# Performance work log

Measured on AMD Instinct MI355X. Metric: run time of the kernel, lower is better.

Reference implementation:

```python
import jax, jax.numpy as jnp
import numpy as np

jax.config.update("jax_enable_x64", True)

B, T, C = 64, 720, 512


def setup_inputs() -> dict:
    key = jax.random.key(0)
    kx, _ = jax.random.split(key)
    x = jax.random.normal(kx, (B, T, C), dtype=jnp.float32)
    # learnable EMA coefficient (scalar parameter)
    alpha = jnp.asarray(0.3, dtype=jnp.float32)
    return {"x": x, "alpha": alpha}


def reference(x, alpha):
    # x: [B, T, C] float32, alpha: scalar float32
    t = x.shape[1]
    alpha_d = alpha.astype(jnp.float64)
    # powers = flip(arange(t)) = [t-1, t-2, ..., 0], double precision as in torch
    powers = jnp.arange(t - 1, -1, -1, dtype=jnp.float64)  # [T]
    base = jnp.power(1.0 - alpha_d, powers)                # (1-a)^(t-1-i), [T]
    divisor = base
    # weights[0] = base[0]; weights[i>=1] = base[i] * alpha
    weights = base * jnp.where(jnp.arange(t) == 0, 1.0, alpha_d)
    # broadcast to [1, T, 1]; compute in float64 (torch promotes f32*f64 -> f64)
    num = jnp.cumsum(x.astype(jnp.float64) * weights[None, :, None], axis=1)
    ma = (num / divisor[None, :, None]).astype(jnp.float32)  # [B, T, C]
    res = x - ma
    return (res, ma)
```

## Files before the change

kernel.cpp:

```cpp
#include <hip/hip_runtime.h>


constexpr int kB  = 64;
constexpr int kT  = 720;
constexpr int kC  = 512;
constexpr int kC4 = kC / 4;
constexpr int kJ  = 16;
constexpr int kL  = 45;
constexpr int kNT = kB * kJ * kC4;

__global__ __launch_bounds__(256, 2) void ema_partials(const float4* __restrict__ x,
                                                       const float* __restrict__ alphap,
                                                       float4* __restrict__ s) {
    const int tid = blockIdx.x * 256 + threadIdx.x;
    const int c   = tid & (kC4 - 1);
    const int bj  = tid >> 7;
    const int j   = bj & (kJ - 1);
    const int b   = bj >> 4;
    const float alpha = alphap[0];
    const float beta  = 1.0f - alpha;

    const float4* xp = x + (size_t)(b * kT + j * kL) * kC4 + c;

    const float4 v0 = xp[0];
    const float w0  = (j == 0) ? 1.0f : alpha;
    float p0 = w0 * v0.x, p1 = w0 * v0.y, p2 = w0 * v0.z, p3 = w0 * v0.w;
    #pragma unroll
    for (int i = 1; i < kL; ++i) {
        const float4 u = xp[i * kC4];
        p0 = fmaf(beta, p0, alpha * u.x);
        p1 = fmaf(beta, p1, alpha * u.y);
        p2 = fmaf(beta, p2, alpha * u.z);
        p3 = fmaf(beta, p3, alpha * u.w);
    }
    s[tid] = make_float4(p0, p1, p2, p3);
}

__global__ __launch_bounds__(256, 2) void ema_apply(const float4* __restrict__ x,
                                                    const float* __restrict__ alphap,
                                                    const float4* __restrict__ s,
                                                    float4* __restrict__ res,
                                                    float4* __restrict__ ma) {
    const int tid = blockIdx.x * 256 + threadIdx.x;
    const int c   = tid & (kC4 - 1);
    const int bj  = tid >> 7;
    const int j   = bj & (kJ - 1);
    const int b   = bj >> 4;
    const float alpha = alphap[0];
    const float beta  = 1.0f - alpha;

    float betaL = 1.0f;
    #pragma unroll
    for (int i = 0; i < kL; ++i) betaL *= beta;

    const float4* sp = s + (size_t)(b * kJ) * kC4 + c;
    float E0 = 0.0f, E1 = 0.0f, E2 = 0.0f, E3 = 0.0f;
    for (int k = 0; k < j; ++k) {
        const float4 sv = sp[k * kC4];
        E0 = fmaf(E0, betaL, sv.x);
        E1 = fmaf(E1, betaL, sv.y);
        E2 = fmaf(E2, betaL, sv.z);
        E3 = fmaf(E3, betaL, sv.w);
    }

    const size_t base = (size_t)(b * kT + j * kL) * kC4 + c;
    const float4* xp = x   + base;
    float4*       rp = res + base;
    float4*       mp = ma  + base;

    {
        const float4 u = xp[0];
        const float w = (j == 0) ? 1.0f : alpha;
        E0 = fmaf(beta, E0, w * u.x);
        E1 = fmaf(beta, E1, w * u.y);
        E2 = fmaf(beta, E2, w * u.z);
        E3 = fmaf(beta, E3, w * u.w);
        mp[0] = make_float4(E0, E1, E2, E3);
        rp[0] = make_float4(u.x - E0, u.y - E1, u.z - E2, u.w - E3);
    }
    #pragma unroll
    for (int i = 1; i < kL; ++i) {
        const float4 u = xp[i * kC4];
        E0 = fmaf(beta, E0, alpha * u.x);
        E1 = fmaf(beta, E1, alpha * u.y);
        E2 = fmaf(beta, E2, alpha * u.z);
        E3 = fmaf(beta, E3, alpha * u.w);
        mp[i * kC4] = make_float4(E0, E1, E2, E3);
        rp[i * kC4] = make_float4(u.x - E0, u.y - E1, u.z - E2, u.w - E3);
    }
}

extern "C" void kernel_launch(void* const* d_in, const int* in_sizes, int n_in,
                              void* d_out, int out_size, void* d_ws, size_t ws_size,
                              hipStream_t stream) {
    const float4* x     = (const float4*)d_in[0];
    const float* alphap = (const float*)d_in[1];
    float4* res = (float4*)d_out;
    float4* ma  = res + (size_t)kB * kT * kC4;
    float4* s   = (float4*)d_ws;

    const int nblk = kNT / 256;
    ema_partials<<<nblk, 256, 0, stream>>>(x, alphap, s);
    ema_apply   <<<nblk, 256, 0, stream>>>(x, alphap, s, res, ma);
}
```

Baseline: 274.0 us.

## Fuse EMA partials and apply into single-pass chained scan with ticket ordering

Replaces the two kernels (chunk partials, then apply) with one kernel where each 64-thread block takes a dynamic ticket to get its (batch, chunk) in order. It computes its chunk partial, publishes it with a release flag, then spin-waits on the earlier chunks' flags before doing the apply pass. Each block now covers all 512 channels (two float4 per lane), and the apply pass reuses the first row it loaded. The second kernel launch goes away, and the x re-read may hit in cache because it happens right after the partial pass. In exchange it adds a memset, atomic spin-waiting, and small 64-thread blocks that may lower occupancy.

```diff
diff --git a/kernel.cpp b/kernel.cpp
--- a/kernel.cpp
+++ b/kernel.cpp
@@ -3,90 +3,95 @@
 
 constexpr int kB  = 64;
 constexpr int kT  = 720;
-constexpr int kC  = 512;
-constexpr int kC4 = kC / 4;
+constexpr int kC4 = 128;
 constexpr int kJ  = 16;
 constexpr int kL  = 45;
-constexpr int kNT = kB * kJ * kC4;
+constexpr int kNB = kB * kJ;
 
-__global__ __launch_bounds__(256, 2) void ema_partials(const float4* __restrict__ x,
-                                                       const float* __restrict__ alphap,
-                                                       float4* __restrict__ s) {
-    const int tid = blockIdx.x * 256 + threadIdx.x;
-    const int c   = tid & (kC4 - 1);
-    const int bj  = tid >> 7;
-    const int j   = bj & (kJ - 1);
-    const int b   = bj >> 4;
+__global__ __launch_bounds__(64) void ema_scan(const float4* __restrict__ x,
+                                               const float*  __restrict__ alphap,
+                                               float4* __restrict__ res,
+                                               float4* __restrict__ ma,
+                                               unsigned* __restrict__ flags,
+                                               unsigned* __restrict__ ticket,
+                                               float4*   __restrict__ s) {
+    const int lane = threadIdx.x;
+
+    unsigned t = 0;
+    if (lane == 0)
+        t = __hip_atomic_fetch_add(ticket, 1u, __ATOMIC_RELAXED, __HIP_MEMORY_SCOPE_AGENT);
+    t = (unsigned)__shfl((int)t, 0);
+    const int b = (int)(t >> 4);
+    const int j = (int)(t & 15u);
+
     const float alpha = alphap[0];
     const float beta  = 1.0f - alpha;
-
-    const float4* xp = x + (size_t)(b * kT + j * kL) * kC4 + c;
-
-    const float4 v0 = xp[0];
-    const float w0  = (j == 0) ? 1.0f : alpha;
-    float p0 = w0 * v0.x, p1 = w0 * v0.y, p2 = w0 * v0.z, p3 = w0 * v0.w;
-    #pragma unroll
-    for (int i = 1; i < kL; ++i) {
-        const float4 u = xp[i * kC4];
-        p0 = fmaf(beta, p0, alpha * u.x);
-        p1 = fmaf(beta, p1, alpha * u.y);
-        p2 = fmaf(beta, p2, alpha * u.z);
-        p3 = fmaf(beta, p3, alpha * u.w);
-    }
-    s[tid] = make_float4(p0, p1, p2, p3);
-}
-
-__global__ __launch_bounds__(256, 2) void ema_apply(const float4* __restrict__ x,
-                                                    const float* __restrict__ alphap,
-                                                    const float4* __restrict__ s,
-                                                    float4* __restrict__ res,
-                                                    float4* __restrict__ ma) {
-    const int tid = blockIdx.x * 256 + threadIdx.x;
-    const int c   = tid & (kC4 - 1);
-    const int bj  = tid >> 7;
-    const int j   = bj & (kJ - 1);
-    const int b   = bj >> 4;
-    const float alpha = alphap[0];
-    const float beta  = 1.0f - alpha;
-
     float betaL = 1.0f;
     #pragma unroll
     for (int i = 0; i < kL; ++i) betaL *= beta;
 
-    const float4* sp = s + (size_t)(b * kJ) * kC4 + c;
-    float E0 = 0.0f, E1 = 0.0f, E2 = 0.0f, E3 = 0.0f;
+    const size_t chunk_base = (size_t)(b * kT + j * kL) * kC4;
+    const float4* xp = x + chunk_base;
+    const int ca = lane, cb = lane + 64;
+
+    const float w0 = (j == 0) ? 1.0f : alpha;
+    const float4 ua = xp[ca], ub = xp[cb];
+    float pa0 = w0*ua.x, pa1 = w0*ua.y, pa2 = w0*ua.z, pa3 = w0*ua.w;
+    float pb0 = w0*ub.x, pb1 = w0*ub.y, pb2 = w0*ub.z, pb3 = w0*ub.w;
+    #pragma unroll
+    for (int i = 1; i < kL; ++i) {
+        const float4 va = xp[i*kC4 + ca];
+        const float4 vb = xp[i*kC4 + cb];
+        pa0 = fmaf(beta, pa0, alpha*va.x); pa1 = fmaf(beta, pa1, alpha*va.y);
+        pa2 = fmaf(beta, pa2, alpha*va.z); pa3 = fmaf(beta, pa3, alpha*va.w);
+        pb0 = fmaf(beta, pb0, alpha*vb.x); pb1 = fmaf(beta, pb1, alpha*vb.y);
+        pb2 = fmaf(beta, pb2, alpha*vb.z); pb3 = fmaf(beta, pb3, alpha*vb.w);
+    }
+    float4* sp = s + (size_t)t * kC4;
+    sp[ca] = make_float4(pa0, pa1, pa2, pa3);
+    sp[cb] = make_float4(pb0, pb1, pb2, pb3);
+    if (lane == 0)
+        __hip_atomic_store(&flags[t], 1u, __ATOMIC_RELEASE, __HIP_MEMORY_SCOPE_AGENT);
+
+    float Ea0 = 0.f, Ea1 = 0.f, Ea2 = 0.f, Ea3 = 0.f;
+    float Eb0 = 0.f, Eb1 = 0.f, Eb2 = 0.f, Eb3 = 0.f;
+    const unsigned fb = t & ~15u;
     for (int k = 0; k < j; ++k) {
-        const float4 sv = sp[k * kC4];
-        E0 = fmaf(E0, betaL, sv.x);
-        E1 = fmaf(E1, betaL, sv.y);
-        E2 = fmaf(E2, betaL, sv.z);
-        E3 = fmaf(E3, betaL, sv.w);
+        while (__hip_atomic_load(&flags[fb + (unsigned)k], __ATOMIC_ACQUIRE,
+                                 __HIP_MEMORY_SCOPE_AGENT) == 0u)
+            __builtin_amdgcn_s_sleep(8);
+        const float4* sk = s + (size_t)(fb + (unsigned)k) * kC4;
+        const float4 sa = sk[ca], sb = sk[cb];
+        Ea0 = fmaf(Ea0, betaL, sa.x); Ea1 = fmaf(Ea1, betaL, sa.y);
+        Ea2 = fmaf(Ea2, betaL, sa.z); Ea3 = fmaf(Ea3, betaL, sa.w);
+        Eb0 = fmaf(Eb0, betaL, sb.x); Eb1 = fmaf(Eb1, betaL, sb.y);
+        Eb2 = fmaf(Eb2, betaL, sb.z); Eb3 = fmaf(Eb3, betaL, sb.w);
     }
 
-    const size_t base = (size_t)(b * kT + j * kL) * kC4 + c;
-    const float4* xp = x   + base;
-    float4*       rp = res + base;
-    float4*       mp = ma  + base;
-
+    float4* rp = res + chunk_base;
+    float4* mp = ma  + chunk_base;
     {
-        const float4 u = xp[0];
-        const float w = (j == 0) ? 1.0f : alpha;
-        E0 = fmaf(beta, E0, w * u.x);
-        E1 = fmaf(beta, E1, w * u.y);
-        E2 = fmaf(beta, E2, w * u.z);
-        E3 = fmaf(beta, E3, w * u.w);
-        mp[0] = make_float4(E0, E1, E2, E3);
-        rp[0] = make_float4(u.x - E0, u.y - E1, u.z - E2, u.w - E3);
+        Ea0 = fmaf(beta, Ea0, w0*ua.x); Ea1 = fmaf(beta, Ea1, w0*ua.y);
+        Ea2 = fmaf(beta, Ea2, w0*ua.z); Ea3 = fmaf(beta, Ea3, w0*ua.w);
+        Eb0 = fmaf(beta, Eb0, w0*ub.x); Eb1 = fmaf(beta, Eb1, w0*ub.y);
+        Eb2 = fmaf(beta, Eb2, w0*ub.z); Eb3 = fmaf(beta, Eb3, w0*ub.w);
+        mp[ca] = make_float4(Ea0, Ea1, Ea2, Ea3);
+        mp[cb] = make_float4(Eb0, Eb1, Eb2, Eb3);
+        rp[ca] = make_float4(ua.x-Ea0, ua.y-Ea1, ua.z-Ea2, ua.w-Ea3);
+        rp[cb] = make_float4(ub.x-Eb0, ub.y-Eb1, ub.z-Eb2, ub.w-Eb3);
     }
     #pragma unroll
     for (int i = 1; i < kL; ++i) {
-        const float4 u = xp[i * kC4];
-        E0 = fmaf(beta, E0, alpha * u.x);
-        E1 = fmaf(beta, E1, alpha * u.y);
-        E2 = fmaf(beta, E2, alpha * u.z);
-        E3 = fmaf(beta, E3, alpha * u.w);
-        mp[i * kC4] = make_float4(E0, E1, E2, E3);
-        rp[i * kC4] = make_float4(u.x - E0, u.y - E1, u.z - E2, u.w - E3);
+        const float4 va = xp[i*kC4 + ca];
+        const float4 vb = xp[i*kC4 + cb];
+        Ea0 = fmaf(beta, Ea0, alpha*va.x); Ea1 = fmaf(beta, Ea1, alpha*va.y);
+        Ea2 = fmaf(beta, Ea2, alpha*va.z); Ea3 = fmaf(beta, Ea3, alpha*va.w);
+        Eb0 = fmaf(beta, Eb0, alpha*vb.x); Eb1 = fmaf(beta, Eb1, alpha*vb.y);
+        Eb2 = fmaf(beta, Eb2, alpha*vb.z); Eb3 = fmaf(beta, Eb3, alpha*vb.w);
+        mp[i*kC4 + ca] = make_float4(Ea0, Ea1, Ea2, Ea3);
+        mp[i*kC4 + cb] = make_float4(Eb0, Eb1, Eb2, Eb3);
+        rp[i*kC4 + ca] = make_float4(va.x-Ea0, va.y-Ea1, va.z-Ea2, va.w-Ea3);
+        rp[i*kC4 + cb] = make_float4(vb.x-Eb0, vb.y-Eb1, vb.z-Eb2, vb.w-Eb3);
     }
 }
 
@@ -97,9 +102,11 @@
     const float* alphap = (const float*)d_in[1];
     float4* res = (float4*)d_out;
     float4* ma  = res + (size_t)kB * kT * kC4;
-    float4* s   = (float4*)d_ws;
 
-    const int nblk = kNT / 256;
-    ema_partials<<<nblk, 256, 0, stream>>>(x, alphap, s);
-    ema_apply   <<<nblk, 256, 0, stream>>>(x, alphap, s, res, ma);
+    unsigned* flags  = (unsigned*)d_ws;
+    unsigned* ticket = flags + kNB;
+    float4*   s      = (float4*)((char*)d_ws + 8192);
+
+    hipMemsetAsync(d_ws, 0, 8192, stream);
+    ema_scan<<<kNB, 64, 0, stream>>>(x, alphap, res, ma, flags, ticket, s);
 }
```

New measurement: 354.8 us. 1.3x slower.
